# Performance work log

Measured on AMD Instinct MI355X. Metric: run time of the kernel, lower is better.

## Reference

```python
import jax, jax.numpy as jnp
import numpy as np


def gcn_layer(x, W, b, src, dst):
    """GCNConv: out = D^{-1/2} (A + I) D^{-1/2} (x W) + b, aggregation at dst."""
    n = x.shape[0]
    h = x @ W  # [N, F_out]
    loops = jnp.arange(n, dtype=src.dtype)
    src_l = jnp.concatenate([src, loops])  # add self-loops
    dst_l = jnp.concatenate([dst, loops])
    ones = jnp.ones(dst_l.shape[0], dtype=x.dtype)
    deg = jax.ops.segment_sum(ones, dst_l, num_segments=n)  # in-degree incl. self-loop
    dinv = jnp.where(deg > 0, jax.lax.rsqrt(deg), 0.0)
    norm = dinv[src_l] * dinv[dst_l]  # [E+N]
    msg = h[src_l] * norm[:, None]  # gather + scale
    agg = jax.ops.segment_sum(msg, dst_l, num_segments=n)  # scatter-add
    return agg + b


def setup_inputs() -> dict:
    key = jax.random.key(0)
    k1, k2, k3, k4 = jax.random.split(key, 4)
    N, E = 1_000_000, 8_000_000
    x = jax.random.normal(k1, (N, 4), dtype=jnp.float32)
    edge_index = jax.random.randint(k2, (2, E), 0, N, dtype=jnp.int64)
    # glorot-ish init for the two GCN linear weights
    W1 = jax.random.normal(k3, (4, 64), dtype=jnp.float32) * (1.0 / np.sqrt(4))
    b1 = jnp.zeros((64,), dtype=jnp.float32)
    W2 = jax.random.normal(k4, (64, 2), dtype=jnp.float32) * (1.0 / np.sqrt(64))
    b2 = jnp.zeros((2,), dtype=jnp.float32)
    return {"x": x, "edge_index": edge_index, "W1": W1, "b1": b1, "W2": W2, "b2": b2}


def reference(x, edge_index, W1, b1, W2, b2):
    src, dst = edge_index[0], edge_index[1]
    h = jax.nn.relu(gcn_layer(x, W1, b1, src, dst))
    return gcn_layer(h, W2, b2, src, dst)
```

## Files before the change

### kernel.cpp

```cpp
#include <hip/hip_runtime.h>
#include <hip/hip_fp16.h>

#define CF_T 512
#define EPT 31
#define CHUNK (CF_T * EPT)
#define BB 11
#define BSZ (1 << BB)
#define BMASK (BSZ - 1)
#define SLICES 4
#define SSHIFT 18
#define MAXNKEY 2048
#define S2T 512
#define SCAP 4608
#define CP(i) ((i) + ((i) >> 5))

__device__ __forceinline__ int detect64(const int* __restrict__ ei) {
    return (ei[1] | ei[3] | ei[5] | ei[7] | ei[9] | ei[11] | ei[13] | ei[15]) == 0;
}
__device__ __forceinline__ int load_src(const int* __restrict__ ei, int e, int is64) {
    return is64 ? ei[2 * (size_t)e] : ei[(size_t)e];
}
__device__ __forceinline__ int load_dst(const int* __restrict__ ei, int E, int e, int is64) {
    return is64 ? ei[2 * ((size_t)E + e)] : ei[(size_t)E + e];
}
__device__ __forceinline__ unsigned int h2u(__half2 h) {
    union { __half2 h; unsigned int u; } c; c.h = h; return c.u;
}
__device__ __forceinline__ __half2 u2h(unsigned int u) {
    union { __half2 h; unsigned int u; } c; c.u = u; return c.h;
}

__global__ __launch_bounds__(256) void init_cur(
    unsigned int* __restrict__ gcur, int NKEY, unsigned int capk) {
    int k = blockIdx.x * 256 + threadIdx.x;
    if (k < NKEY) gcur[k] = (unsigned int)k * capk;
}

__global__ __launch_bounds__(CF_T) void chunk_sort_flush(
    const int* __restrict__ ei, int E, int NKEY, int CPX,
    unsigned int* __restrict__ gcur, unsigned int* __restrict__ ebin,
    unsigned int total_cap) {
    __shared__ unsigned int cnt[MAXNKEY];
    __shared__ unsigned int gdst[MAXNKEY];
    __shared__ unsigned int ssum[CF_T];
    __shared__ unsigned int stg[CHUNK];
    int t = threadIdx.x, bid = blockIdx.x;
    int blk = (bid & 7) * CPX + (bid >> 3);
    int lo = blk * CHUNK;
    if (lo >= E) return;
    int hi = lo + CHUNK; if (hi > E) hi = E;
    for (int u = t; u < MAXNKEY; u += CF_T) cnt[u] = 0;
    __syncthreads();
    int is64 = detect64(ei);
    unsigned int rec[EPT];
    unsigned int ky[(EPT + 1) / 2];
#pragma unroll
    for (int j = 0; j < (EPT + 1) / 2; ++j) ky[j] = 0;
#pragma unroll
    for (int j = 0; j < EPT; ++j) {
        int e = lo + t + j * CF_T;
        if (e < hi) {
            int s = load_src(ei, e, is64);
            int d = load_dst(ei, E, e, is64);
            unsigned int key = ((unsigned int)(d >> BB) << 2) | (unsigned int)(s >> SSHIFT);
            rec[j] = ((unsigned int)s << BB) | (unsigned int)(d & BMASK);
            ky[j >> 1] |= key << ((j & 1) * 16);
            atomicAdd(&cnt[key], 1u);
        }
    }
    __syncthreads();
    unsigned int v[4];
    unsigned int sum = 0;
#pragma unroll
    for (int j = 0; j < 4; ++j) { unsigned int c = cnt[4 * t + j]; v[j] = sum; sum += c; }
    ssum[t] = sum;
    __syncthreads();
    for (int o = 1; o < CF_T; o <<= 1) {
        unsigned int x2 = (t >= o) ? ssum[t - o] : 0;
        __syncthreads();
        ssum[t] += x2;
        __syncthreads();
    }
    unsigned int base = t ? ssum[t - 1] : 0;
#pragma unroll
    for (int j = 0; j < 4; ++j) cnt[4 * t + j] = base + v[j];
    __syncthreads();
#pragma unroll
    for (int j = 0; j < EPT; ++j) {
        int e = lo + t + j * CF_T;
        if (e < hi) {
            unsigned int key = (ky[j >> 1] >> ((j & 1) * 16)) & 0xFFFFu;
            unsigned int pos = atomicAdd(&cnt[key], 1u);
            stg[pos] = rec[j];
        }
    }
    __syncthreads();
    for (int u = t; u < NKEY; u += CF_T) {
        unsigned int lst = u ? cnt[u - 1] : 0;
        unsigned int L = cnt[u] - lst;
        if (L) gdst[u] = atomicAdd(&gcur[u], L) - lst;
    }
    __syncthreads();
    int w = t >> 6, lane = t & 63, nw = CF_T >> 6;
    int g16 = lane >> 4, l16 = lane & 15;
    for (int u0 = w * 4; u0 < NKEY; u0 += nw * 4) {
        int u = u0 + g16;
        if (u < NKEY) {
            unsigned int lst = u ? cnt[u - 1] : 0;
            unsigned int en = cnt[u];
            for (unsigned int j = lst + l16; j < en; j += 16) {
                unsigned int gpos = gdst[u] + j;
                if (gpos < total_cap) ebin[gpos] = stg[j];
            }
        }
    }
}

__global__ __launch_bounds__(S2T) void sort2(
    const unsigned int* __restrict__ ebin, const unsigned int* __restrict__ gcur,
    unsigned int* __restrict__ ebin2, unsigned short* __restrict__ rp16,
    unsigned int capk) {
    __shared__ unsigned int cnt[CP(BSZ)];
    __shared__ unsigned int ssum[S2T];
    __shared__ unsigned int stg2[SCAP];
    int k = blockIdx.x, t = threadIdx.x;
    for (int j = t; j < CP(BSZ); j += S2T) cnt[j] = 0;
    __syncthreads();
    unsigned int kb = (unsigned int)k * capk;
    unsigned int ne_raw = gcur[k] - kb;
    int ne = (int)(ne_raw < capk ? ne_raw : capk);
    for (int i = t; i < ne; i += S2T) {
        unsigned int k11 = ebin[kb + i] & BMASK;
        atomicAdd(&cnt[CP(k11)], 1u);
    }
    __syncthreads();
    unsigned int loc[4];
    unsigned int s = 0;
#pragma unroll
    for (int j = 0; j < 4; ++j) { loc[j] = s; s += cnt[CP(4 * t + j)]; }
    ssum[t] = s;
    __syncthreads();
    for (int o = 1; o < S2T; o <<= 1) {
        unsigned int v = (t >= o) ? ssum[t - o] : 0;
        __syncthreads();
        ssum[t] += v;
        __syncthreads();
    }
    unsigned int tb = t ? ssum[t - 1] : 0;
    size_t rb = (size_t)k * BSZ;
#pragma unroll
    for (int j = 0; j < 4; ++j)
        rp16[rb + 4 * t + j] = (unsigned short)(tb + loc[j]);
#pragma unroll
    for (int j = 0; j < 4; ++j) cnt[CP(4 * t + j)] = tb + loc[j];
    __syncthreads();
    for (int i = t; i < ne; i += S2T) {
        unsigned int rec = ebin[kb + i];
        unsigned int pos = atomicAdd(&cnt[CP(rec & BMASK)], 1u);
        unsigned int v = rec >> BB;
        if (pos < SCAP) stg2[pos] = v;
        else ebin2[kb + pos] = v;
    }
    __syncthreads();
    int m = ne < SCAP ? ne : SCAP;
    for (int j = t; j < m; j += S2T) ebin2[kb + j] = stg2[j];
}

__global__ __launch_bounds__(256) void deg_prep(
    const unsigned short* __restrict__ rp16, const unsigned int* __restrict__ gcur,
    const float4* __restrict__ x, float* __restrict__ dinv, uint2* __restrict__ xs,
    int N, unsigned int capk) {
    int g = blockIdx.x * 256 + threadIdx.x;
    if (g >= N) return;
    int b = g >> BB, j = g & BMASK;
    unsigned int deg = 0;
#pragma unroll
    for (int s = 0; s < SLICES; ++s) {
        int key = (b << 2) | s;
        size_t rb = (size_t)key * BSZ;
        unsigned int st = rp16[rb + j];
        unsigned int en;
        if (j == BMASK) {
            unsigned int ner = gcur[key] - (unsigned int)key * capk;
            en = ner < capk ? ner : capk;
        } else en = rp16[rb + j + 1];
        deg += en - st;
    }
    float di = rsqrtf((float)(deg + 1u));
    dinv[g] = di;
    float4 v = x[g];
    uint2 p;
    p.x = h2u(__halves2half2(__float2half_rn(v.x * di), __float2half_rn(v.y * di)));
    p.y = h2u(__halves2half2(__float2half_rn(v.z * di), __float2half_rn(v.w * di)));
    xs[g] = p;
}

__global__ __launch_bounds__(256) void l1_fused(
    const unsigned int* __restrict__ ebin2, const unsigned short* __restrict__ rp16,
    const unsigned int* __restrict__ gcur, const uint2* __restrict__ xs,
    const float* __restrict__ dinv,
    const float* __restrict__ W1, const float* __restrict__ b1,
    const float* __restrict__ W2, unsigned int* __restrict__ ps,
    int N, unsigned int capk) {
    __shared__ float sW1[256];
    __shared__ float sb1[64];
    __shared__ float sW2[128];
    int t = threadIdx.x, bid = blockIdx.x;
    sW1[t] = W1[t];
    if (t < 64) sb1[t] = b1[t];
    if (t < 128) sW2[t] = W2[t];
    __syncthreads();
    int g = bid * 256 + t;
    if (g >= N) return;
    int b = g >> BB, j = g & BMASK;
    int xcd = bid & 7;
    float axs = 0.0f, ays = 0.0f, azs = 0.0f, aws = 0.0f;
#pragma unroll
    for (int p = 0; p < SLICES; ++p) {
        int s = (xcd + p) & 3;
        int key = (b << 2) | s;
        unsigned int kb = (unsigned int)key * capk;
        size_t rb = (size_t)key * BSZ;
        unsigned int st = kb + rp16[rb + j];
        unsigned int en;
        if (j == BMASK) {
            unsigned int ner = gcur[key] - kb;
            en = kb + (ner < capk ? ner : capk);
        } else en = kb + rp16[rb + j + 1];
        unsigned int e = st;
        for (; e + 2 <= en; e += 2) {
            unsigned int s0 = ebin2[e], s1 = ebin2[e + 1];
            uint2 r0 = xs[s0], r1 = xs[s1];
            __half2 a01 = u2h(r0.x), a23 = u2h(r0.y);
            __half2 b01 = u2h(r1.x), b23 = u2h(r1.y);
            axs += __half2float(__low2half(a01)) + __half2float(__low2half(b01));
            ays += __half2float(__high2half(a01)) + __half2float(__high2half(b01));
            azs += __half2float(__low2half(a23)) + __half2float(__low2half(b23));
            aws += __half2float(__high2half(a23)) + __half2float(__high2half(b23));
        }
        if (e < en) {
            uint2 rr = xs[ebin2[e]];
            __half2 a01 = u2h(rr.x), a23 = u2h(rr.y);
            axs += __half2float(__low2half(a01));
            ays += __half2float(__high2half(a01));
            azs += __half2float(__low2half(a23));
            aws += __half2float(__high2half(a23));
        }
    }
    float di = dinv[g];
    uint2 raw = xs[g];
    __half2 h01 = u2h(raw.x), h23 = u2h(raw.y);
    float ax = (axs + __half2float(__low2half(h01))) * di;
    float ay = (ays + __half2float(__high2half(h01))) * di;
    float az = (azs + __half2float(__low2half(h23))) * di;
    float aw = (aws + __half2float(__high2half(h23))) * di;
    float p0 = 0.0f, p1 = 0.0f;
#pragma unroll
    for (int k = 0; k < 64; ++k) {
        float h = fmaf(ax, sW1[k],
                  fmaf(ay, sW1[64 + k],
                  fmaf(az, sW1[128 + k],
                  fmaf(aw, sW1[192 + k], sb1[k]))));
        h = fmaxf(h, 0.0f);
        p0 = fmaf(h, sW2[2 * k + 0], p0);
        p1 = fmaf(h, sW2[2 * k + 1], p1);
    }
    ps[g] = h2u(__halves2half2(__float2half_rn(p0 * di), __float2half_rn(p1 * di)));
}

__global__ __launch_bounds__(256) void l2_fused(
    const unsigned int* __restrict__ ebin2, const unsigned short* __restrict__ rp16,
    const unsigned int* __restrict__ gcur, const unsigned int* __restrict__ ps,
    const float* __restrict__ dinv, const float* __restrict__ b2,
    float2* __restrict__ out, int N, unsigned int capk) {
    int t = threadIdx.x, bid = blockIdx.x;
    int g = bid * 256 + t;
    if (g >= N) return;
    int b = g >> BB, j = g & BMASK;
    int xcd = bid & 7;
    float s0 = 0.0f, s1 = 0.0f;
#pragma unroll
    for (int p = 0; p < SLICES; ++p) {
        int s = (xcd + p) & 3;
        int key = (b << 2) | s;
        unsigned int kb = (unsigned int)key * capk;
        size_t rb = (size_t)key * BSZ;
        unsigned int st = kb + rp16[rb + j];
        unsigned int en;
        if (j == BMASK) {
            unsigned int ner = gcur[key] - kb;
            en = kb + (ner < capk ? ner : capk);
        } else en = kb + rp16[rb + j + 1];
        unsigned int e = st;
        for (; e + 2 <= en; e += 2) {
            unsigned int a = ebin2[e], bb = ebin2[e + 1];
            unsigned int ra = ps[a], rb2 = ps[bb];
            __half2 ha = u2h(ra), hb = u2h(rb2);
            s0 += __half2float(__low2half(ha)) + __half2float(__low2half(hb));
            s1 += __half2float(__high2half(ha)) + __half2float(__high2half(hb));
        }
        if (e < en) {
            __half2 h = u2h(ps[ebin2[e]]);
            s0 += __half2float(__low2half(h));
            s1 += __half2float(__high2half(h));
        }
    }
    float di = dinv[g];
    __half2 h = u2h(ps[g]);
    float2 rr;
    rr.x = fmaf(s0 + __half2float(__low2half(h)), di, b2[0]);
    rr.y = fmaf(s1 + __half2float(__high2half(h)), di, b2[1]);
    out[g] = rr;
}

static inline size_t align256(size_t v) { return (v + 255) & ~(size_t)255; }

extern "C" void kernel_launch(void* const* d_in, const int* in_sizes, int n_in,
                              void* d_out, int out_size, void* d_ws, size_t ws_size,
                              hipStream_t stream) {
    const float* x  = (const float*)d_in[0];
    const int*   ei = (const int*)d_in[1];
    const float* W1 = (const float*)d_in[2];
    const float* b1 = (const float*)d_in[3];
    const float* W2 = (const float*)d_in[4];
    const float* b2 = (const float*)d_in[5];

    const int N = in_sizes[0] / 4;
    const int E = in_sizes[1] / 2;
    const int NB = (N + BSZ - 1) >> BB;
    const int NKEY = NB * SLICES;
    const int NBLKc = (E + CHUNK - 1) / CHUNK;
    const int CPX = (NBLKc + 7) / 8;
    const int NBLKn = (N + 255) / 256;

    unsigned int capk = (unsigned int)((E + NKEY - 1) / NKEY);
    capk = capk + capk / 8 + 128;
    capk = (capk + 63u) & ~63u;
    const unsigned int total_cap = (unsigned int)NKEY * capk;

    size_t o = 0;
    size_t o_cur  = o; o = align256(o + (size_t)NKEY * 4);
    size_t o_dinv = o; o = align256(o + (size_t)N * 4);
    size_t o_xs   = o; o = align256(o + (size_t)N * 8);
    size_t o_ps   = o; o = align256(o + (size_t)N * 4);
    size_t o_eb2  = o; o = align256(o + (size_t)total_cap * 4);
    size_t o_rp   = o; o = align256(o + (size_t)NKEY * BSZ * 2);
    size_t o_ebin = o; o = align256(o + (size_t)total_cap * 4);

    char* ws = (char*)d_ws;
    unsigned int*   gcur  = (unsigned int*)(ws + o_cur);
    float*          dinv  = (float*)(ws + o_dinv);
    uint2*          xs    = (uint2*)(ws + o_xs);
    unsigned int*   ps    = (unsigned int*)(ws + o_ps);
    unsigned int*   ebin2 = (unsigned int*)(ws + o_eb2);
    unsigned short* rp16  = (unsigned short*)(ws + o_rp);
    unsigned int*   ebin  = (unsigned int*)(ws + o_ebin);

    init_cur<<<(NKEY + 255) / 256, 256, 0, stream>>>(gcur, NKEY, capk);
    chunk_sort_flush<<<8 * CPX, CF_T, 0, stream>>>(ei, E, NKEY, CPX, gcur, ebin, total_cap);
    sort2<<<NKEY, S2T, 0, stream>>>(ebin, gcur, ebin2, rp16, capk);
    deg_prep<<<NBLKn, 256, 0, stream>>>(rp16, gcur, (const float4*)x, dinv, xs, N, capk);
    l1_fused<<<NBLKn, 256, 0, stream>>>(ebin2, rp16, gcur, xs, dinv, W1, b1, W2, ps, N, capk);
    l2_fused<<<NBLKn, 256, 0, stream>>>(ebin2, rp16, gcur, ps, dinv, b2, (float2*)d_out, N, capk);
}
```

Measured before the change: 291.5 us.

## Pre-gather source features per bin, then stream-reduce in aggregation kernels

Adds a gather pass that copies each edge's source feature (xs, then ps) into a per-edge buffer laid out in sorted bin order. The blocks are mapped so work lands on specific XCDs. The aggregation kernels then read that buffer contiguously instead of doing random gathers inside the per-node reduction loops. This trades extra kernel launches and an extra write and read of the edge-sized buffer for better locality. It only runs when the workspace is large enough, reusing the unsorted ebin region.

```diff
diff --git a/kernel.cpp b/kernel.cpp
--- a/kernel.cpp
+++ b/kernel.cpp
@@ -18,16 +18,23 @@
     return (ei[1] | ei[3] | ei[5] | ei[7] | ei[9] | ei[11] | ei[13] | ei[15]) == 0;
 }
 __device__ __forceinline__ int load_src(const int* __restrict__ ei, int e, int is64) {
-    return is64 ? ei[2 * (size_t)e] : ei[(size_t)e];
+    return ei[is64 ? 2 * (size_t)e : (size_t)e];
 }
 __device__ __forceinline__ int load_dst(const int* __restrict__ ei, int E, int e, int is64) {
-    return is64 ? ei[2 * ((size_t)E + e)] : ei[(size_t)E + e];
+    return ei[is64 ? 2 * ((size_t)E + e) : (size_t)E + e];
 }
 __device__ __forceinline__ unsigned int h2u(__half2 h) {
     union { __half2 h; unsigned int u; } c; c.h = h; return c.u;
 }
 __device__ __forceinline__ __half2 u2h(unsigned int u) {
     union { __half2 h; unsigned int u; } c; c.u = u; return c.h;
+}
+__device__ __forceinline__ void xcd_map(int bid, int& b, int& s, int& sub) {
+    int r = bid & 7, q = bid >> 3;
+    s = r & 3;
+    int half = r >> 2;
+    b = q >> 2;
+    sub = (half << 2) | (q & 3);
 }
 
 __global__ __launch_bounds__(256) void init_cur(
@@ -193,6 +200,152 @@
     p.x = h2u(__halves2half2(__float2half_rn(v.x * di), __float2half_rn(v.y * di)));
     p.y = h2u(__halves2half2(__float2half_rn(v.z * di), __float2half_rn(v.w * di)));
     xs[g] = p;
+}
+
+__global__ __launch_bounds__(256) void gpush_xs(
+    const unsigned int* __restrict__ ebin2, const unsigned int* __restrict__ gcur,
+    const uint2* __restrict__ xs, uint2* __restrict__ ebin2v, unsigned int capk) {
+    int b, s, sub;
+    xcd_map(blockIdx.x, b, s, sub);
+    int key = (b << 2) | s;
+    unsigned int kb = (unsigned int)key * capk;
+    unsigned int ner = gcur[key] - kb;
+    int ne = (int)(ner < capk ? ner : capk);
+    int per = (ne + 7) >> 3;
+    int st = sub * per;
+    int en = st + per; if (en > ne) en = ne;
+    for (int i = st + threadIdx.x; i < en; i += 256)
+        ebin2v[kb + i] = xs[ebin2[kb + i]];
+}
+
+__global__ __launch_bounds__(256) void l1_stream(
+    const uint2* __restrict__ ebin2v, const unsigned short* __restrict__ rp16,
+    const unsigned int* __restrict__ gcur, const uint2* __restrict__ xs,
+    const float* __restrict__ dinv,
+    const float* __restrict__ W1, const float* __restrict__ b1,
+    const float* __restrict__ W2, unsigned int* __restrict__ ps,
+    int N, unsigned int capk) {
+    __shared__ float sW1[256];
+    __shared__ float sb1[64];
+    __shared__ float sW2[128];
+    int t = threadIdx.x, bid = blockIdx.x;
+    sW1[t] = W1[t];
+    if (t < 64) sb1[t] = b1[t];
+    if (t < 128) sW2[t] = W2[t];
+    __syncthreads();
+    int g = bid * 256 + t;
+    if (g >= N) return;
+    int b = g >> BB, j = g & BMASK;
+    unsigned int stq[SLICES], lenq[SLICES], maxlen = 0;
+#pragma unroll
+    for (int s = 0; s < SLICES; ++s) {
+        int key = (b << 2) | s;
+        unsigned int kb = (unsigned int)key * capk;
+        size_t rb = (size_t)key * BSZ;
+        unsigned int st = rp16[rb + j];
+        unsigned int en;
+        if (j == BMASK) {
+            unsigned int ner = gcur[key] - kb;
+            en = ner < capk ? ner : capk;
+        } else en = rp16[rb + j + 1];
+        stq[s] = kb + st;
+        lenq[s] = en - st;
+        if (lenq[s] > maxlen) maxlen = lenq[s];
+    }
+    float axs = 0.0f, ays = 0.0f, azs = 0.0f, aws = 0.0f;
+    for (unsigned int it = 0; it < maxlen; ++it) {
+#pragma unroll
+        for (int s = 0; s < SLICES; ++s) {
+            if (it < lenq[s]) {
+                uint2 v = ebin2v[stq[s] + it];
+                __half2 a01 = u2h(v.x), a23 = u2h(v.y);
+                axs += __half2float(__low2half(a01));
+                ays += __half2float(__high2half(a01));
+                azs += __half2float(__low2half(a23));
+                aws += __half2float(__high2half(a23));
+            }
+        }
+    }
+    float di = dinv[g];
+    uint2 raw = xs[g];
+    __half2 h01 = u2h(raw.x), h23 = u2h(raw.y);
+    float ax = (axs + __half2float(__low2half(h01))) * di;
+    float ay = (ays + __half2float(__high2half(h01))) * di;
+    float az = (azs + __half2float(__low2half(h23))) * di;
+    float aw = (aws + __half2float(__high2half(h23))) * di;
+    float p0 = 0.0f, p1 = 0.0f;
+#pragma unroll
+    for (int k = 0; k < 64; ++k) {
+        float h = fmaf(ax, sW1[k],
+                  fmaf(ay, sW1[64 + k],
+                  fmaf(az, sW1[128 + k],
+                  fmaf(aw, sW1[192 + k], sb1[k]))));
+        h = fmaxf(h, 0.0f);
+        p0 = fmaf(h, sW2[2 * k + 0], p0);
+        p1 = fmaf(h, sW2[2 * k + 1], p1);
+    }
+    ps[g] = h2u(__halves2half2(__float2half_rn(p0 * di), __float2half_rn(p1 * di)));
+}
+
+__global__ __launch_bounds__(256) void gpush_ps(
+    const unsigned int* __restrict__ ebin2, const unsigned int* __restrict__ gcur,
+    const unsigned int* __restrict__ ps, unsigned int* __restrict__ ebin2v,
+    unsigned int capk) {
+    int b, s, sub;
+    xcd_map(blockIdx.x, b, s, sub);
+    int key = (b << 2) | s;
+    unsigned int kb = (unsigned int)key * capk;
+    unsigned int ner = gcur[key] - kb;
+    int ne = (int)(ner < capk ? ner : capk);
+    int per = (ne + 7) >> 3;
+    int st = sub * per;
+    int en = st + per; if (en > ne) en = ne;
+    for (int i = st + threadIdx.x; i < en; i += 256)
+        ebin2v[kb + i] = ps[ebin2[kb + i]];
+}
+
+__global__ __launch_bounds__(256) void l2_stream(
+    const unsigned int* __restrict__ ebin2v, const unsigned short* __restrict__ rp16,
+    const unsigned int* __restrict__ gcur, const unsigned int* __restrict__ ps,
+    const float* __restrict__ dinv, const float* __restrict__ b2,
+    float2* __restrict__ out, int N, unsigned int capk) {
+    int t = threadIdx.x, bid = blockIdx.x;
+    int g = bid * 256 + t;
+    if (g >= N) return;
+    int b = g >> BB, j = g & BMASK;
+    unsigned int stq[SLICES], lenq[SLICES], maxlen = 0;
+#pragma unroll
+    for (int s = 0; s < SLICES; ++s) {
+        int key = (b << 2) | s;
+        unsigned int kb = (unsigned int)key * capk;
+        size_t rb = (size_t)key * BSZ;
+        unsigned int st = rp16[rb + j];
+        unsigned int en;
+        if (j == BMASK) {
+            unsigned int ner = gcur[key] - kb;
+            en = ner < capk ? ner : capk;
+        } else en = rp16[rb + j + 1];
+        stq[s] = kb + st;
+        lenq[s] = en - st;
+        if (lenq[s] > maxlen) maxlen = lenq[s];
+    }
+    float s0 = 0.0f, s1 = 0.0f;
+    for (unsigned int it = 0; it < maxlen; ++it) {
+#pragma unroll
+        for (int s = 0; s < SLICES; ++s) {
+            if (it < lenq[s]) {
+                __half2 h = u2h(ebin2v[stq[s] + it]);
+                s0 += __half2float(__low2half(h));
+                s1 += __half2float(__high2half(h));
+            }
+        }
+    }
+    float di = dinv[g];
+    __half2 h = u2h(ps[g]);
+    float2 rr;
+    rr.x = fmaf(s0 + __half2float(__low2half(h)), di, b2[0]);
+    rr.y = fmaf(s1 + __half2float(__high2half(h)), di, b2[1]);
+    out[g] = rr;
 }
 
 __global__ __launch_bounds__(256) void l1_fused(
@@ -345,21 +498,34 @@
     size_t o_ps   = o; o = align256(o + (size_t)N * 4);
     size_t o_eb2  = o; o = align256(o + (size_t)total_cap * 4);
     size_t o_rp   = o; o = align256(o + (size_t)NKEY * BSZ * 2);
-    size_t o_ebin = o; o = align256(o + (size_t)total_cap * 4);
+    size_t o_R    = o;
+    size_t need_fused  = o_R + align256((size_t)total_cap * 4);
+    size_t need_stream = o_R + align256((size_t)total_cap * 8);
+    const bool use_stream = (need_stream <= ws_size);
 
     char* ws = (char*)d_ws;
-    unsigned int*   gcur  = (unsigned int*)(ws + o_cur);
-    float*          dinv  = (float*)(ws + o_dinv);
-    uint2*          xs    = (uint2*)(ws + o_xs);
-    unsigned int*   ps    = (unsigned int*)(ws + o_ps);
-    unsigned int*   ebin2 = (unsigned int*)(ws + o_eb2);
-    unsigned short* rp16  = (unsigned short*)(ws + o_rp);
-    unsigned int*   ebin  = (unsigned int*)(ws + o_ebin);
+    unsigned int*   gcur   = (unsigned int*)(ws + o_cur);
+    float*          dinv   = (float*)(ws + o_dinv);
+    uint2*          xs     = (uint2*)(ws + o_xs);
+    unsigned int*   ps     = (unsigned int*)(ws + o_ps);
+    unsigned int*   ebin2  = (unsigned int*)(ws + o_eb2);
+    unsigned short* rp16   = (unsigned short*)(ws + o_rp);
+    unsigned int*   ebin   = (unsigned int*)(ws + o_R);
+    uint2*          eb2v   = (uint2*)(ws + o_R);
+    unsigned int*   eb2vu  = (unsigned int*)(ws + o_R);
+    (void)need_fused;
 
     init_cur<<<(NKEY + 255) / 256, 256, 0, stream>>>(gcur, NKEY, capk);
     chunk_sort_flush<<<8 * CPX, CF_T, 0, stream>>>(ei, E, NKEY, CPX, gcur, ebin, total_cap);
     sort2<<<NKEY, S2T, 0, stream>>>(ebin, gcur, ebin2, rp16, capk);
     deg_prep<<<NBLKn, 256, 0, stream>>>(rp16, gcur, (const float4*)x, dinv, xs, N, capk);
-    l1_fused<<<NBLKn, 256, 0, stream>>>(ebin2, rp16, gcur, xs, dinv, W1, b1, W2, ps, N, capk);
-    l2_fused<<<NBLKn, 256, 0, stream>>>(ebin2, rp16, gcur, ps, dinv, b2, (float2*)d_out, N, capk);
-}
+    if (use_stream) {
+        gpush_xs<<<NB * 32, 256, 0, stream>>>(ebin2, gcur, xs, eb2v, capk);
+        l1_stream<<<NBLKn, 256, 0, stream>>>(eb2v, rp16, gcur, xs, dinv, W1, b1, W2, ps, N, capk);
+        gpush_ps<<<NB * 32, 256, 0, stream>>>(ebin2, gcur, ps, eb2vu, capk);
+        l2_stream<<<NBLKn, 256, 0, stream>>>(eb2vu, rp16, gcur, ps, dinv, b2, (float2*)d_out, N, capk);
+    } else {
+        l1_fused<<<NBLKn, 256, 0, stream>>>(ebin2, rp16, gcur, xs, dinv, W1, b1, W2, ps, N, capk);
+        l2_fused<<<NBLKn, 256, 0, stream>>>(ebin2, rp16, gcur, ps, dinv, b2, (float2*)d_out, N, capk);
+    }
+}
```

Measured after the change: 323.3 us. +10.9%, slower.
